# Kernel optimization log

Hardware: AMD Instinct MI355X
Metric: run time of the kernel (lower is better)

## Reference

```python
import jax, jax.numpy as jnp
import numpy as np

EMB = 768
HEADS = 12


def setup_inputs() -> dict:
    key = jax.random.key(0)
    ks = jax.random.split(key, 5)
    B, N, E = 8, 1024, EMB
    x = jax.random.normal(ks[0], (B, N, E), dtype=jnp.float32)
    s = 1.0 / np.sqrt(E)
    W_qkv = jax.random.normal(ks[1], (E, 3 * E), dtype=jnp.float32) * s
    b_qkv = jnp.zeros((3 * E,), dtype=jnp.float32)
    W_fc = jax.random.normal(ks[2], (E, E), dtype=jnp.float32) * s
    b_fc = jnp.zeros((E,), dtype=jnp.float32)
    return {"x": x, "W_qkv": W_qkv, "b_qkv": b_qkv, "W_fc": W_fc, "b_fc": b_fc}


def reference(x, W_qkv, b_qkv, W_fc, b_fc):
    B, N, E = x.shape
    H = HEADS
    D = E // H
    qkv = x @ W_qkv + b_qkv                      # [B, N, 3E]
    q, k, v = jnp.split(qkv, 3, axis=-1)
    # b n (h d) -> b h n d
    def to_heads(t):
        return t.reshape(B, N, H, D).transpose(0, 2, 1, 3)
    q, k, v = to_heads(q), to_heads(k), to_heads(v)
    scale = 1.0 / jnp.sqrt(jnp.float32(E))       # NOTE: scales by sqrt(emb_size), not head dim
    attn = jnp.einsum('bhid,bhjd->bhij', q, k) * scale
    attn = jax.nn.softmax(attn, axis=-1)
    out = jnp.einsum('bhij,bhjd->bhid', attn, v)
    out = out.transpose(0, 2, 1, 3).reshape(B, N, E)  # b h n d -> b n (h d)
    return out @ W_fc + b_fc
```

## Files before the change

### kernel.cpp

```cpp
#include <hip/hip_runtime.h>


typedef unsigned short u16;
typedef unsigned int u32;
typedef __attribute__((ext_vector_type(8))) short short8;
typedef __attribute__((ext_vector_type(4))) float f32x4;

#define DEV static __device__ __forceinline__

DEV u16 f2bf(float f) {
  union { float f; u32 u; } v; v.f = f;
  return (u16)((v.u + 0x7FFFu + ((v.u >> 16) & 1u)) >> 16);
}

DEV void gload_lds16(const void* g, void* l) {
  __builtin_amdgcn_global_load_lds(
      (const __attribute__((address_space(1))) void*)g,
      (__attribute__((address_space(3))) void*)l, 16, 0, 0);
}

__global__ void cvt_bf16_kernel(const float* __restrict__ in, u16* __restrict__ out, int n8) {
  int idx = blockIdx.x * blockDim.x + threadIdx.x;
  int stride = gridDim.x * blockDim.x;
  for (int i = idx; i < n8; i += stride) {
    float4 a = reinterpret_cast<const float4*>(in)[2 * i];
    float4 b = reinterpret_cast<const float4*>(in)[2 * i + 1];
    uint4 o;
    o.x = f2bf(a.x) | ((u32)f2bf(a.y) << 16);
    o.y = f2bf(a.z) | ((u32)f2bf(a.w) << 16);
    o.z = f2bf(b.x) | ((u32)f2bf(b.y) << 16);
    o.w = f2bf(b.z) | ((u32)f2bf(b.w) << 16);
    reinterpret_cast<uint4*>(out)[i] = o;
  }
}

__global__ void trcvt_kernel(const float* __restrict__ in, u16* __restrict__ out,
                             int K, int Nn) {
  __shared__ u16 tile[64][72];
  int ntiles = Nn >> 6;
  int tk = blockIdx.x / ntiles, tn = blockIdx.x % ntiles;
  int k0 = tk << 6, n0 = tn << 6;
  int t = threadIdx.x;
  int r = t >> 4;
  int c4 = (t & 15) << 2;
#pragma unroll
  for (int ps = 0; ps < 4; ++ps) {
    int k = r + ps * 16;
    float4 v = *reinterpret_cast<const float4*>(&in[(size_t)(k0 + k) * Nn + n0 + c4]);
    tile[c4 + 0][k] = f2bf(v.x);
    tile[c4 + 1][k] = f2bf(v.y);
    tile[c4 + 2][k] = f2bf(v.z);
    tile[c4 + 3][k] = f2bf(v.w);
  }
  __syncthreads();
  int nr = t >> 3;
  int c8 = (t & 7) << 3;
#pragma unroll
  for (int ps = 0; ps < 2; ++ps) {
    int n = nr + ps * 32;
    uint4 v = *reinterpret_cast<const uint4*>(&tile[n][c8]);
    *reinterpret_cast<uint4*>(&out[(size_t)(n0 + n) * K + k0 + c8]) = v;
  }
}

__global__ void trv_kernel(const u16* __restrict__ vh, u16* __restrict__ vt) {
  __shared__ u16 tile[64][72];
  int nt = blockIdx.x & 15;
  int bh = blockIdx.x >> 4;
  int n0 = nt << 6;
  int t = threadIdx.x;
  int nr = t >> 3;
  int d8 = (t & 7) << 3;
  const u16* src = vh + ((size_t)bh * 1024 + n0) * 64;
#pragma unroll
  for (int ps = 0; ps < 2; ++ps) {
    int n = nr + ps * 32;
    uint4 v = *reinterpret_cast<const uint4*>(&src[(size_t)n * 64 + d8]);
    const u16* e = reinterpret_cast<const u16*>(&v);
#pragma unroll
    for (int j = 0; j < 8; ++j) tile[d8 + j][n] = e[j];
  }
  __syncthreads();
  u16* dst = vt + ((size_t)bh * 64) * 1024 + n0;
#pragma unroll
  for (int ps = 0; ps < 2; ++ps) {
    int d = nr + ps * 32;
    uint4 v = *reinterpret_cast<const uint4*>(&tile[d][d8]);
    *reinterpret_cast<uint4*>(&dst[(size_t)d * 1024 + d8]) = v;
  }
}

template <int MODE>
__global__ __launch_bounds__(256, 4) void gemm_bt(
    const u16* __restrict__ A, const u16* __restrict__ Bt,
    const float* __restrict__ bias, void* __restrict__ Cout,
    u16* __restrict__ qh, u16* __restrict__ kh, u16* __restrict__ vh,
    int Nn) {
  __shared__ u16 As[128 * 32];
  __shared__ u16 Bs[128 * 32];
  const int nTn = Nn >> 7;
  const int nwg = gridDim.x;
  int wg = blockIdx.x;
  wg = (wg & 7) * (nwg >> 3) + (wg >> 3);
  const int tm = wg / nTn, tn = wg % nTn;
  const int m0 = tm << 7, n0 = tn << 7;
  const int tid = threadIdx.x;
  const int w = tid >> 6, lane = tid & 63;
  const int g = lane >> 4, p = lane & 15;
  const int wr = w >> 1, wc = w & 1;

  const int srow = lane >> 2;
  const int schunk = (lane & 3) ^ ((srow >> 1) & 3);
  const u16* Asrc = A + (size_t)(m0 + srow) * 768 + schunk * 8;
  const u16* Bsrc = Bt + (size_t)(n0 + srow) * 768 + schunk * 8;
  const int csw = (g ^ ((p >> 1) & 3)) << 3;

  f32x4 acc[4][4] = {};

  for (int kt = 0; kt < 768; kt += 32) {
#pragma unroll
    for (int i = 0; i < 2; ++i) {
      int trow = w * 32 + i * 16;
      gload_lds16(Asrc + (size_t)trow * 768 + kt, &As[trow * 32]);
      gload_lds16(Bsrc + (size_t)trow * 768 + kt, &Bs[trow * 32]);
    }
    __syncthreads();
    short8 af[4], bf[4];
#pragma unroll
    for (int mb = 0; mb < 4; ++mb)
      af[mb] = *reinterpret_cast<const short8*>(&As[(wr * 64 + mb * 16 + p) * 32 + csw]);
#pragma unroll
    for (int nb = 0; nb < 4; ++nb)
      bf[nb] = *reinterpret_cast<const short8*>(&Bs[(wc * 64 + nb * 16 + p) * 32 + csw]);
#pragma unroll
    for (int mb = 0; mb < 4; ++mb)
#pragma unroll
      for (int nb = 0; nb < 4; ++nb)
        acc[mb][nb] = __builtin_amdgcn_mfma_f32_16x16x32_bf16(af[mb], bf[nb], acc[mb][nb], 0, 0, 0);
    __syncthreads();
  }

  const float qscale = 0.036084391824351615f;
#pragma unroll
  for (int nb = 0; nb < 4; ++nb) {
    int ncol = n0 + wc * 64 + nb * 16 + p;
    float bv = bias[ncol];
    if (MODE == 0) {
#pragma unroll
      for (int mb = 0; mb < 4; ++mb)
#pragma unroll
        for (int r = 0; r < 4; ++r) {
          int m = m0 + wr * 64 + mb * 16 + g * 4 + r;
          ((float*)Cout)[(size_t)m * Nn + ncol] = acc[mb][nb][r] + bv;
        }
    } else {
      int h64 = ncol >> 6;
      int which = h64 / 12;
      int hh = h64 - which * 12;
      int d = ncol & 63;
      u16* dst = which == 0 ? qh : (which == 1 ? kh : vh);
      float sc = which == 0 ? qscale : 1.f;
#pragma unroll
      for (int mb = 0; mb < 4; ++mb)
#pragma unroll
        for (int r = 0; r < 4; ++r) {
          int m = m0 + wr * 64 + mb * 16 + g * 4 + r;
          int bb = m >> 10, nr = m & 1023;
          dst[(((size_t)bb * 12 + hh) * 1024 + nr) * 64 + d] = f2bf((acc[mb][nb][r] + bv) * sc);
        }
    }
  }
}

__global__ __launch_bounds__(512, 6) void attn_kernel(
    const u16* __restrict__ qh, const u16* __restrict__ kh,
    const u16* __restrict__ vt, u16* __restrict__ ao) {
  __shared__ u16 Ks[2][64 * 64];
  __shared__ u16 Vs[2][64 * 64];
  __shared__ u16 Ps[8][16 * 64];
  const int bid = blockIdx.x;
  const int qt = bid & 7;
  const int bh = bid >> 3;
  const int b = bh / 12, h = bh % 12;
  const int tid = threadIdx.x;
  const int w = tid >> 6, lane = tid & 63;
  const int g = lane >> 4, p = lane & 15;
  const int qrow = qt * 128 + w * 16;

  const u16* qbase = qh + ((size_t)bh * 1024 + qrow + p) * 64;
  short8 qf0 = *reinterpret_cast<const short8*>(qbase + g * 8);
  short8 qf1 = *reinterpret_cast<const short8*>(qbase + 32 + g * 8);

  const int ci = w * 64 + lane;
  const int crow = ci >> 3;
  const int csw = (ci & 7) ^ (crow & 7);
  const u16* ksrc = kh + (((size_t)bh * 1024 + crow) << 6) + csw * 8;
  const u16* vsrc = vt + ((size_t)bh * 64 + crow) * 1024 + csw * 8;
  u16* myp = Ps[w];

  const int sw = p & 7;
  const int c0 = (g ^ sw) << 3;
  const int c1 = ((4 + g) ^ sw) << 3;

  float m_run = -1e30f, l_run = 0.f;
  f32x4 oacc[4] = {};

  gload_lds16(ksrc, &Ks[0][w * 512]);
  gload_lds16(vsrc, &Vs[0][w * 512]);
  __syncthreads();

  int buf = 0;
  for (int kt = 0; kt < 1024; kt += 64) {
    if (kt < 960) {
      gload_lds16(ksrc + ((kt + 64) << 6), &Ks[buf ^ 1][w * 512]);
      gload_lds16(vsrc + (kt + 64), &Vs[buf ^ 1][w * 512]);
    }

    f32x4 s[4];
    __builtin_amdgcn_s_setprio(1);
#pragma unroll
    for (int jb = 0; jb < 4; ++jb) {
      const u16* kb = &Ks[buf][(jb * 16 + p) * 64];
      short8 k0 = *reinterpret_cast<const short8*>(kb + c0);
      short8 k1 = *reinterpret_cast<const short8*>(kb + c1);
      f32x4 z = {};
      z = __builtin_amdgcn_mfma_f32_16x16x32_bf16(k0, qf0, z, 0, 0, 0);
      z = __builtin_amdgcn_mfma_f32_16x16x32_bf16(k1, qf1, z, 0, 0, 0);
      s[jb] = z;
    }
    __builtin_amdgcn_s_setprio(0);

    float tmax = -1e30f;
#pragma unroll
    for (int jb = 0; jb < 4; ++jb)
#pragma unroll
      for (int r = 0; r < 4; ++r) tmax = fmaxf(tmax, s[jb][r]);
    tmax = fmaxf(tmax, __shfl_xor(tmax, 16));
    tmax = fmaxf(tmax, __shfl_xor(tmax, 32));
    float m_new = fmaxf(m_run, tmax);
    float alpha = __expf(m_run - m_new);
    float lsum = 0.f;
#pragma unroll
    for (int jb = 0; jb < 4; ++jb)
#pragma unroll
      for (int r = 0; r < 4; ++r) {
        float e = __expf(s[jb][r] - m_new);
        s[jb][r] = e;
        lsum += e;
      }
    lsum += __shfl_xor(lsum, 16);
    lsum += __shfl_xor(lsum, 32);
    l_run = l_run * alpha + lsum;
    m_run = m_new;

#pragma unroll
    for (int jb = 0; jb < 4; ++jb) {
      uint2 pk;
      pk.x = f2bf(s[jb][0]) | ((u32)f2bf(s[jb][1]) << 16);
      pk.y = f2bf(s[jb][2]) | ((u32)f2bf(s[jb][3]) << 16);
      int c = 2 * jb + (g >> 1);
      *reinterpret_cast<uint2*>(&myp[p * 64 + ((c ^ sw) << 3) + ((g & 1) << 2)]) = pk;
    }

    float al[4];
#pragma unroll
    for (int r = 0; r < 4; ++r) al[r] = __shfl(alpha, g * 4 + r);
#pragma unroll
    for (int nb = 0; nb < 4; ++nb)
#pragma unroll
      for (int r = 0; r < 4; ++r) oacc[nb][r] *= al[r];

    short8 pa0 = *reinterpret_cast<const short8*>(&myp[p * 64 + c0]);
    short8 pa1 = *reinterpret_cast<const short8*>(&myp[p * 64 + c1]);
    __builtin_amdgcn_s_setprio(1);
#pragma unroll
    for (int nb = 0; nb < 4; ++nb) {
      const u16* vb = &Vs[buf][(nb * 16 + p) * 64];
      short8 v0 = *reinterpret_cast<const short8*>(vb + c0);
      short8 v1 = *reinterpret_cast<const short8*>(vb + c1);
      oacc[nb] = __builtin_amdgcn_mfma_f32_16x16x32_bf16(pa0, v0, oacc[nb], 0, 0, 0);
      oacc[nb] = __builtin_amdgcn_mfma_f32_16x16x32_bf16(pa1, v1, oacc[nb], 0, 0, 0);
    }
    __builtin_amdgcn_s_setprio(0);

    __syncthreads();
    buf ^= 1;
  }

  float li[4];
#pragma unroll
  for (int r = 0; r < 4; ++r) li[r] = 1.f / __shfl(l_run, g * 4 + r);
  u16* obase = ao + ((size_t)(b * 1024 + qrow)) * 768 + h * 64;
#pragma unroll
  for (int nb = 0; nb < 4; ++nb)
#pragma unroll
    for (int r = 0; r < 4; ++r)
      obase[(size_t)(g * 4 + r) * 768 + nb * 16 + p] = f2bf(oacc[nb][r] * li[r]);
}

extern "C" void kernel_launch(void* const* d_in, const int* in_sizes, int n_in,
                              void* d_out, int out_size, void* d_ws, size_t ws_size,
                              hipStream_t stream) {
  const float* x = (const float*)d_in[0];
  const float* Wqkv = (const float*)d_in[1];
  const float* bqkv = (const float*)d_in[2];
  const float* Wfc = (const float*)d_in[3];
  const float* bfc = (const float*)d_in[4];
  float* out = (float*)d_out;

  char* ws = (char*)d_ws;
  u16* xb    = (u16*)(ws);
  u16* wqkvT = (u16*)(ws + 12582912);
  u16* wfcT  = (u16*)(ws + 16121856);
  u16* qh    = (u16*)(ws + 17301504);
  u16* kh    = (u16*)(ws + 29884416);
  u16* vh    = (u16*)(ws + 42467328);
  u16* vt    = (u16*)(ws + 55050240);
  u16* ao    = (u16*)(ws + 67633152);

  cvt_bf16_kernel<<<2048, 256, 0, stream>>>(x, xb, (8192 * 768) / 8);
  trcvt_kernel<<<12 * 36, 256, 0, stream>>>(Wqkv, wqkvT, 768, 2304);
  trcvt_kernel<<<12 * 12, 256, 0, stream>>>(Wfc, wfcT, 768, 768);
  gemm_bt<2><<<64 * 18, 256, 0, stream>>>(xb, wqkvT, bqkv, nullptr, qh, kh, vh, 2304);
  trv_kernel<<<96 * 16, 256, 0, stream>>>(vh, vt);
  attn_kernel<<<96 * 8, 512, 0, stream>>>(qh, kh, vt, ao);
  gemm_bt<0><<<64 * 6, 256, 0, stream>>>(ao, wfcT, bfc, out, nullptr, nullptr, nullptr, 768);
}
```

Measured before the change: 141.7 us.

## Rewrite GEMMs as 256x256 double-buffered 8-wave pipelined kernel, fuse V transpose

Replaces the 128x128 single-buffer GEMM with a 256x256 tile, 512-thread kernel that uses double-buffered LDS with 64-wide K steps. Global-to-LDS loads are interleaved with MFMA phases under explicit barriers, waitcnts and setprio. The QKV epilogue now writes V directly in transposed layout, which removes the separate trv_kernel launch. Risks include strided scattered 2-byte stores for V, fewer workgroups (96 for the FC GEMM, fewer than the CU count), and much higher register and LDS use.

```diff
diff --git a/kernel.cpp b/kernel.cpp
--- a/kernel.cpp
+++ b/kernel.cpp
@@ -63,82 +63,118 @@
   }
 }
 
-__global__ void trv_kernel(const u16* __restrict__ vh, u16* __restrict__ vt) {
-  __shared__ u16 tile[64][72];
-  int nt = blockIdx.x & 15;
-  int bh = blockIdx.x >> 4;
-  int n0 = nt << 6;
-  int t = threadIdx.x;
-  int nr = t >> 3;
-  int d8 = (t & 7) << 3;
-  const u16* src = vh + ((size_t)bh * 1024 + n0) * 64;
-#pragma unroll
-  for (int ps = 0; ps < 2; ++ps) {
-    int n = nr + ps * 32;
-    uint4 v = *reinterpret_cast<const uint4*>(&src[(size_t)n * 64 + d8]);
-    const u16* e = reinterpret_cast<const u16*>(&v);
-#pragma unroll
-    for (int j = 0; j < 8; ++j) tile[d8 + j][n] = e[j];
-  }
-  __syncthreads();
-  u16* dst = vt + ((size_t)bh * 64) * 1024 + n0;
-#pragma unroll
-  for (int ps = 0; ps < 2; ++ps) {
-    int d = nr + ps * 32;
-    uint4 v = *reinterpret_cast<const uint4*>(&tile[d][d8]);
-    *reinterpret_cast<uint4*>(&dst[(size_t)d * 1024 + d8]) = v;
-  }
-}
-
 template <int MODE>
-__global__ __launch_bounds__(256, 4) void gemm_bt(
+__global__ __launch_bounds__(512, 2) void gemm8p(
     const u16* __restrict__ A, const u16* __restrict__ Bt,
     const float* __restrict__ bias, void* __restrict__ Cout,
-    u16* __restrict__ qh, u16* __restrict__ kh, u16* __restrict__ vh,
+    u16* __restrict__ qh, u16* __restrict__ kh, u16* __restrict__ vt,
     int Nn) {
-  __shared__ u16 As[128 * 32];
-  __shared__ u16 Bs[128 * 32];
-  const int nTn = Nn >> 7;
+  __shared__ u16 As[2][256 * 64];
+  __shared__ u16 Bs[2][256 * 64];
+  const int nTn = Nn >> 8;
   const int nwg = gridDim.x;
   int wg = blockIdx.x;
   wg = (wg & 7) * (nwg >> 3) + (wg >> 3);
   const int tm = wg / nTn, tn = wg % nTn;
-  const int m0 = tm << 7, n0 = tn << 7;
+  const int m0 = tm << 8, n0 = tn << 8;
   const int tid = threadIdx.x;
   const int w = tid >> 6, lane = tid & 63;
   const int g = lane >> 4, p = lane & 15;
-  const int wr = w >> 1, wc = w & 1;
-
-  const int srow = lane >> 2;
-  const int schunk = (lane & 3) ^ ((srow >> 1) & 3);
-  const u16* Asrc = A + (size_t)(m0 + srow) * 768 + schunk * 8;
-  const u16* Bsrc = Bt + (size_t)(n0 + srow) * 768 + schunk * 8;
-  const int csw = (g ^ ((p >> 1) & 3)) << 3;
-
-  f32x4 acc[4][4] = {};
-
-  for (int kt = 0; kt < 768; kt += 32) {
-#pragma unroll
-    for (int i = 0; i < 2; ++i) {
-      int trow = w * 32 + i * 16;
-      gload_lds16(Asrc + (size_t)trow * 768 + kt, &As[trow * 32]);
-      gload_lds16(Bsrc + (size_t)trow * 768 + kt, &Bs[trow * 32]);
-    }
-    __syncthreads();
-    short8 af[4], bf[4];
-#pragma unroll
-    for (int mb = 0; mb < 4; ++mb)
-      af[mb] = *reinterpret_cast<const short8*>(&As[(wr * 64 + mb * 16 + p) * 32 + csw]);
-#pragma unroll
-    for (int nb = 0; nb < 4; ++nb)
-      bf[nb] = *reinterpret_cast<const short8*>(&Bs[(wc * 64 + nb * 16 + p) * 32 + csw]);
-#pragma unroll
-    for (int mb = 0; mb < 4; ++mb)
-#pragma unroll
-      for (int nb = 0; nb < 4; ++nb)
-        acc[mb][nb] = __builtin_amdgcn_mfma_f32_16x16x32_bf16(af[mb], bf[nb], acc[mb][nb], 0, 0, 0);
-    __syncthreads();
-  }
+  const int wr = w >> 2, wc = w & 3;
+
+  const int srow8 = lane >> 3;
+  const int sch = (lane & 7) ^ srow8;
+  const u16* Abase = A + (size_t)(m0 + w * 16 + srow8) * 768 + sch * 8;
+  const u16* Bbase = Bt + (size_t)(n0 + w * 16 + srow8) * 768 + sch * 8;
+  const int ldsrow = w * 16;
+  const int c0 = (g ^ (p & 7)) << 3;
+  const int c1 = ((4 + g) ^ (p & 7)) << 3;
+
+  f32x4 acc[8][4] = {};
+  short8 af[4][2], bf[4][2];
+
+#define STG(Xbase, XS, h, kt, bi)                                              \
+  do {                                                                         \
+    gload_lds16(Xbase + (size_t)((h) * 128) * 768 + (kt) * 64,                 \
+                &XS[bi][((h) * 128 + ldsrow) * 64]);                           \
+    gload_lds16(Xbase + (size_t)((h) * 128 + 8) * 768 + (kt) * 64,             \
+                &XS[bi][((h) * 128 + ldsrow + 8) * 64]);                       \
+  } while (0)
+
+#define RDA(moff, cb)                                                          \
+  _Pragma("unroll") for (int mb = 0; mb < 4; ++mb) {                           \
+    const u16* ra = &As[cb][(wr * 128 + (moff) + mb * 16 + p) * 64];           \
+    af[mb][0] = *reinterpret_cast<const short8*>(ra + c0);                     \
+    af[mb][1] = *reinterpret_cast<const short8*>(ra + c1);                     \
+  }
+
+#define RDB(nbase, cb)                                                         \
+  _Pragma("unroll") for (int nn = 0; nn < 2; ++nn) {                           \
+    const u16* rb = &Bs[cb][(wc * 64 + (nbase) * 16 + nn * 16 + p) * 64];      \
+    bf[(nbase) + nn][0] = *reinterpret_cast<const short8*>(rb + c0);           \
+    bf[(nbase) + nn][1] = *reinterpret_cast<const short8*>(rb + c1);           \
+  }
+
+#define MM(mo, no)                                                             \
+  _Pragma("unroll") for (int mb = 0; mb < 4; ++mb)                             \
+  _Pragma("unroll") for (int nn = 0; nn < 2; ++nn) {                           \
+    acc[(mo) + mb][(no) + nn] = __builtin_amdgcn_mfma_f32_16x16x32_bf16(       \
+        af[mb][0], bf[(no) + nn][0], acc[(mo) + mb][(no) + nn], 0, 0, 0);      \
+    acc[(mo) + mb][(no) + nn] = __builtin_amdgcn_mfma_f32_16x16x32_bf16(       \
+        af[mb][1], bf[(no) + nn][1], acc[(mo) + mb][(no) + nn], 0, 0, 0);      \
+  }
+
+  STG(Abase, As, 0, 0, 0); STG(Abase, As, 1, 0, 0);
+  STG(Bbase, Bs, 0, 0, 0); STG(Bbase, Bs, 1, 0, 0);
+  STG(Abase, As, 0, 1, 1);
+  asm volatile("s_waitcnt vmcnt(2)");
+  __builtin_amdgcn_sched_barrier(0);
+  __builtin_amdgcn_s_barrier();
+
+#pragma unroll
+  for (int t = 0; t < 12; ++t) {
+    const int cb = t & 1, nb_ = cb ^ 1;
+    RDA(0, cb)
+    RDB(0, cb)
+    if (t + 1 < 12) STG(Abase, As, 1, t + 1, nb_);
+    __builtin_amdgcn_s_barrier();
+    asm volatile("s_waitcnt lgkmcnt(0)");
+    __builtin_amdgcn_sched_barrier(0);
+    __builtin_amdgcn_s_setprio(1);
+    MM(0, 0)
+    __builtin_amdgcn_s_setprio(0);
+    __builtin_amdgcn_s_barrier();
+    RDB(2, cb)
+    if (t + 1 < 12) STG(Bbase, Bs, 0, t + 1, nb_);
+    __builtin_amdgcn_s_barrier();
+    asm volatile("s_waitcnt lgkmcnt(0)");
+    __builtin_amdgcn_sched_barrier(0);
+    __builtin_amdgcn_s_setprio(1);
+    MM(0, 2)
+    __builtin_amdgcn_s_setprio(0);
+    __builtin_amdgcn_s_barrier();
+    RDA(64, cb)
+    if (t + 1 < 12) STG(Bbase, Bs, 1, t + 1, nb_);
+    __builtin_amdgcn_s_barrier();
+    asm volatile("s_waitcnt lgkmcnt(0)");
+    __builtin_amdgcn_sched_barrier(0);
+    __builtin_amdgcn_s_setprio(1);
+    MM(4, 0)
+    __builtin_amdgcn_s_setprio(0);
+    __builtin_amdgcn_s_barrier();
+    if (t + 2 < 12) STG(Abase, As, 0, t + 2, cb);
+    __builtin_amdgcn_s_setprio(1);
+    MM(4, 2)
+    __builtin_amdgcn_s_setprio(0);
+    if (t < 10) asm volatile("s_waitcnt vmcnt(2)");
+    else if (t == 10) asm volatile("s_waitcnt vmcnt(0)");
+    __builtin_amdgcn_sched_barrier(0);
+    __builtin_amdgcn_s_barrier();
+  }
+#undef STG
+#undef RDA
+#undef RDB
+#undef MM
 
   const float qscale = 0.036084391824351615f;
 #pragma unroll
@@ -147,10 +183,10 @@
     float bv = bias[ncol];
     if (MODE == 0) {
 #pragma unroll
-      for (int mb = 0; mb < 4; ++mb)
+      for (int mb = 0; mb < 8; ++mb)
 #pragma unroll
         for (int r = 0; r < 4; ++r) {
-          int m = m0 + wr * 64 + mb * 16 + g * 4 + r;
+          int m = m0 + wr * 128 + mb * 16 + g * 4 + r;
           ((float*)Cout)[(size_t)m * Nn + ncol] = acc[mb][nb][r] + bv;
         }
     } else {
@@ -158,15 +194,20 @@
       int which = h64 / 12;
       int hh = h64 - which * 12;
       int d = ncol & 63;
-      u16* dst = which == 0 ? qh : (which == 1 ? kh : vh);
-      float sc = which == 0 ? qscale : 1.f;
-#pragma unroll
-      for (int mb = 0; mb < 4; ++mb)
+#pragma unroll
+      for (int mb = 0; mb < 8; ++mb)
 #pragma unroll
         for (int r = 0; r < 4; ++r) {
-          int m = m0 + wr * 64 + mb * 16 + g * 4 + r;
+          int m = m0 + wr * 128 + mb * 16 + g * 4 + r;
           int bb = m >> 10, nr = m & 1023;
-          dst[(((size_t)bb * 12 + hh) * 1024 + nr) * 64 + d] = f2bf((acc[mb][nb][r] + bv) * sc);
+          float vv = acc[mb][nb][r] + bv;
+          if (which == 2) {
+            vt[((size_t)(bb * 12 + hh) * 64 + d) * 1024 + nr] = f2bf(vv);
+          } else {
+            u16* dst = which == 0 ? qh : kh;
+            float sc = which == 0 ? qscale : 1.f;
+            dst[(((size_t)bb * 12 + hh) * 1024 + nr) * 64 + d] = f2bf(vv * sc);
+          }
         }
     }
   }
@@ -314,15 +355,13 @@
   u16* wfcT  = (u16*)(ws + 16121856);
   u16* qh    = (u16*)(ws + 17301504);
   u16* kh    = (u16*)(ws + 29884416);
-  u16* vh    = (u16*)(ws + 42467328);
   u16* vt    = (u16*)(ws + 55050240);
   u16* ao    = (u16*)(ws + 67633152);
 
   cvt_bf16_kernel<<<2048, 256, 0, stream>>>(x, xb, (8192 * 768) / 8);
   trcvt_kernel<<<12 * 36, 256, 0, stream>>>(Wqkv, wqkvT, 768, 2304);
   trcvt_kernel<<<12 * 12, 256, 0, stream>>>(Wfc, wfcT, 768, 768);
-  gemm_bt<2><<<64 * 18, 256, 0, stream>>>(xb, wqkvT, bqkv, nullptr, qh, kh, vh, 2304);
-  trv_kernel<<<96 * 16, 256, 0, stream>>>(vh, vt);
+  gemm8p<2><<<288, 512, 0, stream>>>(xb, wqkvT, bqkv, nullptr, qh, kh, vt, 2304);
   attn_kernel<<<96 * 8, 512, 0, stream>>>(qh, kh, vt, ao);
-  gemm_bt<0><<<64 * 6, 256, 0, stream>>>(ao, wfcT, bfc, out, nullptr, nullptr, nullptr, 768);
-}
+  gemm8p<0><<<96, 512, 0, stream>>>(ao, wfcT, bfc, out, nullptr, nullptr, nullptr, 768);
+}
```

New measurement: 171.2 us. 20.8% more time.

## Deepen GEMM and attention LDS pipelines to four-stage async prefetch

Applied to the files above, without the earlier changes.

Both the projection GEMM and the attention kernel move from a single or double LDS buffer to a 4-slot ring that prefetches 3 tiles ahead. Explicit vmcnt waits with raw barriers replace __syncthreads, so global-to-LDS loads overlap with MFMA work. The GEMM also raises MFMA priority with setprio. In exchange LDS use grows and launch-bound occupancy drops (4→2 and 6→2 blocks per CU), which cuts latency hiding through wave parallelism.

```diff
diff --git a/kernel.cpp b/kernel.cpp
--- a/kernel.cpp
+++ b/kernel.cpp
@@ -91,13 +91,13 @@
 }
 
 template <int MODE>
-__global__ __launch_bounds__(256, 4) void gemm_bt(
+__global__ __launch_bounds__(256, 2) void gemm_bt(
     const u16* __restrict__ A, const u16* __restrict__ Bt,
     const float* __restrict__ bias, void* __restrict__ Cout,
     u16* __restrict__ qh, u16* __restrict__ kh, u16* __restrict__ vh,
     int Nn) {
-  __shared__ u16 As[128 * 32];
-  __shared__ u16 Bs[128 * 32];
+  __shared__ u16 As[4][128 * 32];
+  __shared__ u16 Bs[4][128 * 32];
   const int nTn = Nn >> 7;
   const int nwg = gridDim.x;
   int wg = blockIdx.x;
@@ -117,28 +117,50 @@
 
   f32x4 acc[4][4] = {};
 
-  for (int kt = 0; kt < 768; kt += 32) {
-#pragma unroll
-    for (int i = 0; i < 2; ++i) {
-      int trow = w * 32 + i * 16;
-      gload_lds16(Asrc + (size_t)trow * 768 + kt, &As[trow * 32]);
-      gload_lds16(Bsrc + (size_t)trow * 768 + kt, &Bs[trow * 32]);
-    }
-    __syncthreads();
+#define STAGE(kt, sbuf)                                                          \
+  do {                                                                           \
+    _Pragma("unroll")                                                            \
+    for (int i = 0; i < 2; ++i) {                                                \
+      int trow = w * 32 + i * 16;                                                \
+      gload_lds16(Asrc + (size_t)trow * 768 + (size_t)(kt) * 32,                 \
+                  &As[sbuf][trow * 32]);                                         \
+      gload_lds16(Bsrc + (size_t)trow * 768 + (size_t)(kt) * 32,                 \
+                  &Bs[sbuf][trow * 32]);                                         \
+    }                                                                            \
+  } while (0)
+
+  STAGE(0, 0);
+  STAGE(1, 1);
+  STAGE(2, 2);
+  asm volatile("s_waitcnt vmcnt(8)" ::: "memory");
+  __builtin_amdgcn_s_barrier();
+  __builtin_amdgcn_sched_barrier(0);
+
+  for (int k = 0; k < 24; ++k) {
+    const u16* as = As[k & 3];
+    const u16* bs = Bs[k & 3];
+    if (k < 21) STAGE(k + 3, (k + 3) & 3);
     short8 af[4], bf[4];
 #pragma unroll
     for (int mb = 0; mb < 4; ++mb)
-      af[mb] = *reinterpret_cast<const short8*>(&As[(wr * 64 + mb * 16 + p) * 32 + csw]);
+      af[mb] = *reinterpret_cast<const short8*>(&as[(wr * 64 + mb * 16 + p) * 32 + csw]);
 #pragma unroll
     for (int nb = 0; nb < 4; ++nb)
-      bf[nb] = *reinterpret_cast<const short8*>(&Bs[(wc * 64 + nb * 16 + p) * 32 + csw]);
+      bf[nb] = *reinterpret_cast<const short8*>(&bs[(wc * 64 + nb * 16 + p) * 32 + csw]);
+    __builtin_amdgcn_s_setprio(1);
 #pragma unroll
     for (int mb = 0; mb < 4; ++mb)
 #pragma unroll
       for (int nb = 0; nb < 4; ++nb)
         acc[mb][nb] = __builtin_amdgcn_mfma_f32_16x16x32_bf16(af[mb], bf[nb], acc[mb][nb], 0, 0, 0);
-    __syncthreads();
-  }
+    __builtin_amdgcn_s_setprio(0);
+    if (k < 21) asm volatile("s_waitcnt vmcnt(8)" ::: "memory");
+    else if (k == 21) asm volatile("s_waitcnt vmcnt(4)" ::: "memory");
+    else if (k == 22) asm volatile("s_waitcnt vmcnt(0)" ::: "memory");
+    __builtin_amdgcn_s_barrier();
+    __builtin_amdgcn_sched_barrier(0);
+  }
+#undef STAGE
 
   const float qscale = 0.036084391824351615f;
 #pragma unroll
@@ -172,11 +194,11 @@
   }
 }
 
-__global__ __launch_bounds__(512, 6) void attn_kernel(
+__global__ __launch_bounds__(512, 2) void attn_kernel(
     const u16* __restrict__ qh, const u16* __restrict__ kh,
     const u16* __restrict__ vt, u16* __restrict__ ao) {
-  __shared__ u16 Ks[2][64 * 64];
-  __shared__ u16 Vs[2][64 * 64];
+  __shared__ u16 Ks[4][64 * 64];
+  __shared__ u16 Vs[4][64 * 64];
   __shared__ u16 Ps[8][16 * 64];
   const int bid = blockIdx.x;
   const int qt = bid & 7;
@@ -193,9 +215,9 @@
 
   const int ci = w * 64 + lane;
   const int crow = ci >> 3;
-  const int csw = (ci & 7) ^ (crow & 7);
-  const u16* ksrc = kh + (((size_t)bh * 1024 + crow) << 6) + csw * 8;
-  const u16* vsrc = vt + ((size_t)bh * 64 + crow) * 1024 + csw * 8;
+  const int csw2 = (ci & 7) ^ (crow & 7);
+  const u16* ksrc = kh + (((size_t)bh * 1024 + crow) << 6) + csw2 * 8;
+  const u16* vsrc = vt + ((size_t)bh * 64 + crow) * 1024 + csw2 * 8;
   u16* myp = Ps[w];
 
   const int sw = p & 7;
@@ -205,22 +227,28 @@
   float m_run = -1e30f, l_run = 0.f;
   f32x4 oacc[4] = {};
 
-  gload_lds16(ksrc, &Ks[0][w * 512]);
-  gload_lds16(vsrc, &Vs[0][w * 512]);
-  __syncthreads();
-
-  int buf = 0;
-  for (int kt = 0; kt < 1024; kt += 64) {
-    if (kt < 960) {
-      gload_lds16(ksrc + ((kt + 64) << 6), &Ks[buf ^ 1][w * 512]);
-      gload_lds16(vsrc + (kt + 64), &Vs[buf ^ 1][w * 512]);
+#pragma unroll
+  for (int t = 0; t < 3; ++t) {
+    gload_lds16(ksrc + ((size_t)t << 12), &Ks[t][w * 512]);
+    gload_lds16(vsrc + ((size_t)t << 6), &Vs[t][w * 512]);
+  }
+  asm volatile("s_waitcnt vmcnt(4)" ::: "memory");
+  __builtin_amdgcn_s_barrier();
+  __builtin_amdgcn_sched_barrier(0);
+
+  for (int it = 0; it < 16; ++it) {
+    const u16* kbuf = Ks[it & 3];
+    const u16* vbuf = Vs[it & 3];
+    if (it < 13) {
+      gload_lds16(ksrc + ((size_t)(it + 3) << 12), &Ks[(it + 3) & 3][w * 512]);
+      gload_lds16(vsrc + ((size_t)(it + 3) << 6), &Vs[(it + 3) & 3][w * 512]);
     }
 
     f32x4 s[4];
     __builtin_amdgcn_s_setprio(1);
 #pragma unroll
     for (int jb = 0; jb < 4; ++jb) {
-      const u16* kb = &Ks[buf][(jb * 16 + p) * 64];
+      const u16* kb = &kbuf[(jb * 16 + p) * 64];
       short8 k0 = *reinterpret_cast<const short8*>(kb + c0);
       short8 k1 = *reinterpret_cast<const short8*>(kb + c1);
       f32x4 z = {};
@@ -275,7 +303,7 @@
     __builtin_amdgcn_s_setprio(1);
 #pragma unroll
     for (int nb = 0; nb < 4; ++nb) {
-      const u16* vb = &Vs[buf][(nb * 16 + p) * 64];
+      const u16* vb = &vbuf[(nb * 16 + p) * 64];
       short8 v0 = *reinterpret_cast<const short8*>(vb + c0);
       short8 v1 = *reinterpret_cast<const short8*>(vb + c1);
       oacc[nb] = __builtin_amdgcn_mfma_f32_16x16x32_bf16(pa0, v0, oacc[nb], 0, 0, 0);
@@ -283,8 +311,11 @@
     }
     __builtin_amdgcn_s_setprio(0);
 
-    __syncthreads();
-    buf ^= 1;
+    if (it < 13) asm volatile("s_waitcnt vmcnt(4)" ::: "memory");
+    else if (it == 13) asm volatile("s_waitcnt vmcnt(2)" ::: "memory");
+    else if (it == 14) asm volatile("s_waitcnt vmcnt(0)" ::: "memory");
+    __builtin_amdgcn_s_barrier();
+    __builtin_amdgcn_sched_barrier(0);
   }
 
   float li[4];
```

New measurement: 158.7 us. 1.12x slower.
